# Performance work log

Hardware: AMD Instinct MI355X
Metric: run time of the kernel (lower is better)

## Reference

```python
import jax, jax.numpy as jnp
import numpy as np

N, E = 50000, 800000
IN_DIM, HID, HEADS, EDGE_DIM, OUT_DIM = 329, 64, 4, 2, 1
NEG_SLOPE = 0.2


def setup_inputs() -> dict:
    key = jax.random.key(0)
    ks = jax.random.split(key, 20)
    p = lambda k, shp: (jax.random.normal(k, shp, dtype=jnp.float32) * 0.1)
    inp = {
        'x': jax.random.normal(ks[0], (N, IN_DIM), dtype=jnp.float32),
        'edge_attr': jax.random.normal(ks[1], (E, EDGE_DIM), dtype=jnp.float32),
        'edge_index': jax.random.randint(ks[2], (2, E), 0, N, dtype=jnp.int32),
        # conv1: GATConv(329 -> 64, heads=4, edge_dim=2), concat=True
        'W1': p(ks[3], (IN_DIM, HEADS * HID)),
        'att_src1': p(ks[4], (HEADS, HID)),
        'att_dst1': p(ks[5], (HEADS, HID)),
        'We1': p(ks[6], (EDGE_DIM, HEADS * HID)),
        'att_e1': p(ks[7], (HEADS, HID)),
        'b1': jnp.zeros((HEADS * HID,), jnp.float32),
        # conv2: GATConv(256 -> 64, heads=1, edge_dim=2), concat=True
        'W2': p(ks[8], (HEADS * HID, HID)),
        'att_src2': p(ks[9], (1, HID)),
        'att_dst2': p(ks[10], (1, HID)),
        'We2': p(ks[11], (EDGE_DIM, HID)),
        'att_e2': p(ks[12], (1, HID)),
        'b2': jnp.zeros((HID,), jnp.float32),
        # fc head
        'Wf': p(ks[13], (HID, OUT_DIM)),
        'bf': jnp.zeros((OUT_DIM,), jnp.float32),
    }
    return inp


def gat_conv(x, src, dst, ea, W, att_src, att_dst, We, att_e, bias, heads, out_ch):
    n = x.shape[0]
    h = (x @ W).reshape(n, heads, out_ch)                    # [N,H,C]
    a_src = (h * att_src).sum(-1)                            # [N,H]
    a_dst = (h * att_dst).sum(-1)                            # [N,H]
    e = (ea @ We).reshape(-1, heads, out_ch)                 # [Et,H,C]
    a_e = (e * att_e).sum(-1)                                # [Et,H]
    alpha = a_src[src] + a_dst[dst] + a_e                    # [Et,H]
    alpha = jnp.where(alpha > 0, alpha, NEG_SLOPE * alpha)   # leaky_relu
    amax = jax.ops.segment_max(alpha, dst, num_segments=n)
    ex = jnp.exp(alpha - amax[dst])
    denom = jax.ops.segment_sum(ex, dst, num_segments=n)
    attn = ex / (denom[dst] + 1e-16)                         # [Et,H]
    out = jax.ops.segment_sum(attn[..., None] * h[src], dst, num_segments=n)
    return out.reshape(n, heads * out_ch) + bias


def reference(x, edge_attr, edge_index, W1, att_src1, att_dst1, We1, att_e1, b1,
              W2, att_src2, att_dst2, We2, att_e2, b2, Wf, bf):
    n = x.shape[0]
    # add_self_loops with fill_value='mean' for edge_attr (PyG GATConv default)
    loop = jnp.arange(n, dtype=edge_index.dtype)
    src = jnp.concatenate([edge_index[0], loop])
    dst = jnp.concatenate([edge_index[1], loop])
    mean_ea = jnp.mean(edge_attr, axis=0)
    ea = jnp.concatenate([edge_attr, jnp.broadcast_to(mean_ea, (n, edge_attr.shape[1]))])
    h = gat_conv(x, src, dst, ea, W1, att_src1, att_dst1, We1, att_e1, b1, HEADS, HID)
    h = jax.nn.elu(h)
    h = gat_conv(h, src, dst, ea, W2, att_src2, att_dst2, We2, att_e2, b2, 1, HID)
    out = h @ Wf + bf
    return out.squeeze(-1)
```

## Files before the change

kernel.cpp:

```cpp
#include <hip/hip_runtime.h>
#include <hip/hip_bf16.h>
#include <math.h>


#define DEVFN __device__ __forceinline__

typedef __attribute__((ext_vector_type(8))) short short8;
typedef __attribute__((ext_vector_type(4))) float f32x4;

DEVFN float wave_reduce_sum(float v) {
    for (int off = 32; off; off >>= 1) v += __shfl_xor(v, off);
    return v;
}

DEVFN ushort f2bf_rne(float f) {
    unsigned u = __float_as_uint(f);
    unsigned r = (u + 0x7fff + ((u >> 16) & 1)) >> 16;
    return (ushort)r;
}
DEVFN float bf2f(ushort b) { return __uint_as_float(((unsigned)b) << 16); }

__global__ void k_init(int* __restrict__ deg, float* __restrict__ meanbuf, int N) {
    int i = blockIdx.x * blockDim.x + threadIdx.x;
    if (i < N) deg[i] = 0;
    if (i < 2) meanbuf[i] = 0.f;
}

__global__ void k_count(const int* __restrict__ dstrow, int* __restrict__ deg, int E, int Et) {
    int t = blockIdx.x * blockDim.x + threadIdx.x;
    if (t >= Et) return;
    int d = (t < E) ? dstrow[t] : (t - E);
    atomicAdd(&deg[d], 1);
}

__global__ void k_scan_block(const int* __restrict__ deg, int* __restrict__ rowptr,
                             int* __restrict__ bsums, int N) {
    __shared__ int sd[1024];
    int i = blockIdx.x * 1024 + threadIdx.x;
    sd[threadIdx.x] = (i < N) ? deg[i] : 0;
    __syncthreads();
    for (int off = 1; off < 1024; off <<= 1) {
        int x = (threadIdx.x >= off) ? sd[threadIdx.x - off] : 0;
        __syncthreads();
        sd[threadIdx.x] += x;
        __syncthreads();
    }
    if (i < N) rowptr[i + 1] = sd[threadIdx.x];
    if (threadIdx.x == 1023) bsums[blockIdx.x] = sd[1023];
}

__global__ void k_scan_bsums(const int* __restrict__ bsums, int* __restrict__ boffs, int nb) {
    if (threadIdx.x == 0 && blockIdx.x == 0) {
        int run = 0;
        for (int b = 0; b < nb; b++) { boffs[b] = run; run += bsums[b]; }
    }
}

__global__ void k_scan_finalize(int* __restrict__ rowptr, const int* __restrict__ boffs, int N) {
    int i = blockIdx.x * blockDim.x + threadIdx.x;
    if (i < N) rowptr[i + 1] += boffs[i >> 10];
    if (i == 0) rowptr[0] = 0;
}

__global__ void k_copy_cursor(const int* __restrict__ rowptr, int* __restrict__ cursor, int N) {
    int i = blockIdx.x * blockDim.x + threadIdx.x;
    if (i < N) cursor[i] = rowptr[i];
}

__global__ void k_mean(const float* __restrict__ ea, float* __restrict__ meanbuf, int E) {
    __shared__ float s0s[4], s1s[4];
    float s0 = 0.f, s1 = 0.f;
    for (int i = blockIdx.x * blockDim.x + threadIdx.x; i < E; i += gridDim.x * blockDim.x) {
        float2 v = reinterpret_cast<const float2*>(ea)[i];
        s0 += v.x; s1 += v.y;
    }
    s0 = wave_reduce_sum(s0);
    s1 = wave_reduce_sum(s1);
    int lane = threadIdx.x & 63, w = threadIdx.x >> 6;
    if (lane == 0) { s0s[w] = s0; s1s[w] = s1; }
    __syncthreads();
    if (threadIdx.x == 0) {
        float a = 0.f, b = 0.f;
        for (int i = 0; i < (int)(blockDim.x >> 6); i++) { a += s0s[i]; b += s1s[i]; }
        atomicAdd(&meanbuf[0], a);
        atomicAdd(&meanbuf[1], b);
    }
}

__global__ void k_fill(const int* __restrict__ srcrow, const int* __restrict__ dstrow,
                       int* __restrict__ cursor, int* __restrict__ srcid,
                       float2* __restrict__ ea_csr, const float* __restrict__ ea,
                       const float* __restrict__ meanbuf, float invE, int E, int Et) {
    int t = blockIdx.x * blockDim.x + threadIdx.x;
    if (t >= Et) return;
    int d, s; float2 ev;
    if (t < E) {
        d = dstrow[t]; s = srcrow[t];
        ev = reinterpret_cast<const float2*>(ea)[t];
    } else {
        d = t - E; s = t - E;
        ev = make_float2(meanbuf[0] * invE, meanbuf[1] * invE);
    }
    int pos = atomicAdd(&cursor[d], 1);
    srcid[pos] = s;
    ea_csr[pos] = ev;
}

template <int H>
__global__ void k_collapse(const float* __restrict__ We, const float* __restrict__ att_e,
                           float* __restrict__ M) {
    int t = threadIdx.x;
    int lane = t & 63, w = t >> 6;
    int d = w / H, h = w % H;
    float v = We[(d * H + h) * 64 + lane] * att_e[h * 64 + lane];
    v = wave_reduce_sum(v);
    if (lane == 0) M[d * H + h] = v;
}

__global__ void k_split_wT(const float* __restrict__ W, ushort* __restrict__ hiT,
                           ushort* __restrict__ loT, int K, int Nc, int Kpad) {
    int c = blockIdx.x;
    for (int k = threadIdx.x; k < Kpad; k += blockDim.x) {
        float v = (k < K) ? W[(size_t)k * Nc + c] : 0.f;
        ushort h = f2bf_rne(v);
        ushort l = f2bf_rne(v - bf2f(h));
        hiT[(size_t)c * Kpad + k] = h;
        loT[(size_t)c * Kpad + k] = l;
    }
}

template <int MI, int NI>
__global__ __launch_bounds__(256) void k_gemm_mfma(const float* __restrict__ A,
                                                   const ushort* __restrict__ BhT,
                                                   const ushort* __restrict__ BlT,
                                                   float* __restrict__ C,
                                                   int M, int K, int Kpad, int ldc) {
    constexpr int BM = 32 * MI, BN = 32 * NI;
    constexpr int LDA = 40;
    __shared__ __align__(16) ushort Ah[BM * LDA];
    __shared__ __align__(16) ushort Al[BM * LDA];
    __shared__ __align__(16) ushort Bh[BN * LDA];
    __shared__ __align__(16) ushort Bl[BN * LDA];

    int tid = threadIdx.x, lane = tid & 63, wid = tid >> 6;
    int wr = wid >> 1, wc = wid & 1;
    int bm = blockIdx.x * BM, bn = blockIdx.y * BN;

    f32x4 acc[MI][NI];
#pragma unroll
    for (int mi = 0; mi < MI; ++mi)
#pragma unroll
        for (int ni = 0; ni < NI; ++ni) acc[mi][ni] = (f32x4){0.f, 0.f, 0.f, 0.f};

    int steps = Kpad / 32;
    for (int s = 0; s < steps; ++s) {
        int k0 = s * 32;
        __syncthreads();
#pragma unroll
        for (int j = 0; j < BM / 32; ++j) {
            int slot = tid + 256 * j;
            int row = slot >> 3, ch = slot & 7;
            int gr = bm + row, kb = k0 + ch * 4;
            float v[4];
#pragma unroll
            for (int e = 0; e < 4; ++e) {
                int kk = kb + e;
                v[e] = (gr < M && kk < K) ? A[(size_t)gr * K + kk] : 0.f;
            }
            ushort h[4], l[4];
#pragma unroll
            for (int e = 0; e < 4; ++e) {
                h[e] = f2bf_rne(v[e]);
                l[e] = f2bf_rne(v[e] - bf2f(h[e]));
            }
            *reinterpret_cast<ushort4*>(&Ah[row * LDA + ch * 4]) = make_ushort4(h[0], h[1], h[2], h[3]);
            *reinterpret_cast<ushort4*>(&Al[row * LDA + ch * 4]) = make_ushort4(l[0], l[1], l[2], l[3]);
        }
#pragma unroll
        for (int j = 0; j < BN / 64; ++j) {
            int slot = tid + 256 * j;
            int n = slot >> 2, ch = slot & 3;
            size_t goff = (size_t)(bn + n) * Kpad + k0 + ch * 8;
            *reinterpret_cast<float4*>(&Bh[n * LDA + ch * 8]) =
                *reinterpret_cast<const float4*>(&BhT[goff]);
            *reinterpret_cast<float4*>(&Bl[n * LDA + ch * 8]) =
                *reinterpret_cast<const float4*>(&BlT[goff]);
        }
        __syncthreads();
        int kg = (lane >> 4) * 8;
        int am = wr * (MI * 16) + (lane & 15);
        int bc = wc * (NI * 16) + (lane & 15);
        short8 ah[MI], al[MI], bh[NI], bl[NI];
#pragma unroll
        for (int mi = 0; mi < MI; ++mi) {
            ah[mi] = *reinterpret_cast<const short8*>(&Ah[(am + mi * 16) * LDA + kg]);
            al[mi] = *reinterpret_cast<const short8*>(&Al[(am + mi * 16) * LDA + kg]);
        }
#pragma unroll
        for (int ni = 0; ni < NI; ++ni) {
            bh[ni] = *reinterpret_cast<const short8*>(&Bh[(bc + ni * 16) * LDA + kg]);
            bl[ni] = *reinterpret_cast<const short8*>(&Bl[(bc + ni * 16) * LDA + kg]);
        }
#pragma unroll
        for (int mi = 0; mi < MI; ++mi)
#pragma unroll
            for (int ni = 0; ni < NI; ++ni) {
                acc[mi][ni] = __builtin_amdgcn_mfma_f32_16x16x32_bf16(ah[mi], bh[ni], acc[mi][ni], 0, 0, 0);
                acc[mi][ni] = __builtin_amdgcn_mfma_f32_16x16x32_bf16(ah[mi], bl[ni], acc[mi][ni], 0, 0, 0);
                acc[mi][ni] = __builtin_amdgcn_mfma_f32_16x16x32_bf16(al[mi], bh[ni], acc[mi][ni], 0, 0, 0);
            }
    }
#pragma unroll
    for (int mi = 0; mi < MI; ++mi) {
        int row0 = bm + wr * (MI * 16) + mi * 16 + ((lane >> 4) << 2);
#pragma unroll
        for (int ni = 0; ni < NI; ++ni) {
            int col = bn + wc * (NI * 16) + ni * 16 + (lane & 15);
            f32x4 v = acc[mi][ni];
#pragma unroll
            for (int r = 0; r < 4; ++r)
                if (row0 + r < M) C[(size_t)(row0 + r) * ldc + col] = v[r];
        }
    }
}

template <int H>
__global__ void k_node_attn(const float* __restrict__ h, const float* __restrict__ att_src,
                            const float* __restrict__ att_dst, float* __restrict__ asrc,
                            float* __restrict__ adst, int N) {
    constexpr int HC = H * 64;
    constexpr int NPB = 256 / HC;
    int local = threadIdx.x % HC;
    int n = blockIdx.x * NPB + threadIdx.x / HC;
    if (n >= N) return;
    float v = h[(size_t)n * HC + local];
    float s = v * att_src[local];
    float d = v * att_dst[local];
    for (int off = 32; off; off >>= 1) { s += __shfl_xor(s, off); d += __shfl_xor(d, off); }
    if ((local & 63) == 0) {
        int hh = local >> 6;
        asrc[n * H + hh] = s;
        adst[n * H + hh] = d;
    }
}

template <int H>
__global__ void k_attn(const int* __restrict__ rowptr, const int* __restrict__ srcid,
                       const float2* __restrict__ ea_csr, const float* __restrict__ asrc,
                       const float* __restrict__ adst, const float* __restrict__ M,
                       float* __restrict__ attn, float* __restrict__ dinv, int N) {
    int lane = threadIdx.x & 63;
    int n = blockIdx.x * 4 + (threadIdx.x >> 6);
    if (n >= N) return;
    int start = rowptr[n];
    int items = (rowptr[n + 1] - start) * H;
    int h = lane % H;
    float ad = adst[n * H + h];
    float m0 = M[h], m1 = M[H + h];

    float mx = -1e30f;
    for (int i = lane; i < items; i += 64) {
        int p = start + i / H;
        int s = srcid[p];
        float2 ev = ea_csr[p];
        float al = asrc[s * H + h] + ad + ev.x * m0 + ev.y * m1;
        al = (al > 0.f) ? al : 0.2f * al;
        attn[(size_t)start * H + i] = al;
        mx = fmaxf(mx, al);
    }
    for (int off = H; off < 64; off <<= 1) mx = fmaxf(mx, __shfl_xor(mx, off));

    float ss = 0.f;
    for (int i = lane; i < items; i += 64) {
        float ex = expf(attn[(size_t)start * H + i] - mx);
        attn[(size_t)start * H + i] = ex;
        ss += ex;
    }
    for (int off = H; off < 64; off <<= 1) ss += __shfl_xor(ss, off);
    if (lane < H) dinv[n * H + h] = 1.f / (ss + 1e-16f);
}

template <int H, bool ELU>
__global__ void k_aggregate(const int* __restrict__ rowptr, const int* __restrict__ srcid,
                            const float* __restrict__ attn, const float* __restrict__ dinv,
                            const float4* __restrict__ h4, const float* __restrict__ bias,
                            float4* __restrict__ out4, int N) {
    constexpr int LPN = H * 16;
    constexpr int NPB = 256 / LPN;
    int li = threadIdx.x % LPN;
    int n = blockIdx.x * NPB + threadIdx.x / LPN;
    if (n >= N) return;
    int hh = li >> 4;
    int start = rowptr[n], end = rowptr[n + 1];
    float4 acc = make_float4(0.f, 0.f, 0.f, 0.f);
    int p = start;
    for (; p + 3 < end; p += 4) {
        int s0 = srcid[p], s1 = srcid[p + 1], s2 = srcid[p + 2], s3 = srcid[p + 3];
        float w0 = attn[p * H + hh], w1 = attn[(p + 1) * H + hh];
        float w2 = attn[(p + 2) * H + hh], w3 = attn[(p + 3) * H + hh];
        float4 v0 = h4[(size_t)s0 * LPN + li];
        float4 v1 = h4[(size_t)s1 * LPN + li];
        float4 v2 = h4[(size_t)s2 * LPN + li];
        float4 v3 = h4[(size_t)s3 * LPN + li];
        acc.x += w0 * v0.x + w1 * v1.x + w2 * v2.x + w3 * v3.x;
        acc.y += w0 * v0.y + w1 * v1.y + w2 * v2.y + w3 * v3.y;
        acc.z += w0 * v0.z + w1 * v1.z + w2 * v2.z + w3 * v3.z;
        acc.w += w0 * v0.w + w1 * v1.w + w2 * v2.w + w3 * v3.w;
    }
    for (; p < end; ++p) {
        int s = srcid[p];
        float w = attn[p * H + hh];
        float4 v = h4[(size_t)s * LPN + li];
        acc.x += w * v.x; acc.y += w * v.y; acc.z += w * v.z; acc.w += w * v.w;
    }
    float inv = dinv[n * H + hh];
    float4 b = reinterpret_cast<const float4*>(bias)[li];
    acc.x = acc.x * inv + b.x;
    acc.y = acc.y * inv + b.y;
    acc.z = acc.z * inv + b.z;
    acc.w = acc.w * inv + b.w;
    if (ELU) {
        acc.x = (acc.x > 0.f) ? acc.x : expm1f(acc.x);
        acc.y = (acc.y > 0.f) ? acc.y : expm1f(acc.y);
        acc.z = (acc.z > 0.f) ? acc.z : expm1f(acc.z);
        acc.w = (acc.w > 0.f) ? acc.w : expm1f(acc.w);
    }
    out4[(size_t)n * LPN + li] = acc;
}

__global__ void k_fc(const float* __restrict__ h, const float* __restrict__ Wf,
                     const float* __restrict__ bf, float* __restrict__ out, int N) {
    int lane = threadIdx.x & 63;
    int n = blockIdx.x * 4 + (threadIdx.x >> 6);
    if (n >= N) return;
    float v = h[(size_t)n * 64 + lane] * Wf[lane];
    v = wave_reduce_sum(v);
    if (lane == 0) out[n] = v + bf[0];
}

extern "C" void kernel_launch(void* const* d_in, const int* in_sizes, int n_in,
                              void* d_out, int out_size, void* d_ws, size_t ws_size,
                              hipStream_t stream) {
    const float* x        = (const float*)d_in[0];
    const float* ea       = (const float*)d_in[1];
    const int*   ei       = (const int*)d_in[2];
    const float* W1       = (const float*)d_in[3];
    const float* att_src1 = (const float*)d_in[4];
    const float* att_dst1 = (const float*)d_in[5];
    const float* We1      = (const float*)d_in[6];
    const float* att_e1   = (const float*)d_in[7];
    const float* b1       = (const float*)d_in[8];
    const float* W2       = (const float*)d_in[9];
    const float* att_src2 = (const float*)d_in[10];
    const float* att_dst2 = (const float*)d_in[11];
    const float* We2      = (const float*)d_in[12];
    const float* att_e2   = (const float*)d_in[13];
    const float* b2       = (const float*)d_in[14];
    const float* Wf       = (const float*)d_in[15];
    const float* bf       = (const float*)d_in[16];

    const int IN_DIM = 329;
    const int K1PAD = 352;
    int N  = in_sizes[0] / IN_DIM;
    int E  = in_sizes[1] / 2;
    int Et = E + N;
    const int* srcrow = ei;
    const int* dstrow = ei + E;

    char* p = (char*)d_ws;
    size_t used = 0;
    auto alloc = [&](size_t bytes) -> void* {
        void* r = p;
        size_t pad = (bytes + 255) & ~(size_t)255;
        p += pad; used += pad;
        return r;
    };
    float*  h1     = (float*)alloc((size_t)N * 256 * 4);
    float*  agg1   = (float*)alloc((size_t)N * 256 * 4);
    float*  asrc   = (float*)alloc((size_t)N * 4 * 4);
    float*  adst   = (float*)alloc((size_t)N * 4 * 4);
    float*  dinv   = (float*)alloc((size_t)N * 4 * 4);
    float*  attn   = (float*)alloc((size_t)Et * 4 * 4);
    float2* ea_csr = (float2*)alloc((size_t)Et * 8);
    int*    srcid  = (int*)alloc((size_t)Et * 4);
    ushort* w1hT   = (ushort*)alloc((size_t)256 * K1PAD * 2);
    ushort* w1lT   = (ushort*)alloc((size_t)256 * K1PAD * 2);
    ushort* w2hT   = (ushort*)alloc((size_t)64 * 256 * 2);
    ushort* w2lT   = (ushort*)alloc((size_t)64 * 256 * 2);
    float*  M1     = (float*)alloc(256);
    float*  M2     = (float*)alloc(256);
    float*  meanbuf= (float*)alloc(256);
    int*    rowptr = (int*)alloc((size_t)(N + 1) * 4);
    int*    deg    = (int*)alloc((size_t)N * 4);
    int*    bsums  = (int*)alloc(1024);
    int*    boffs  = (int*)alloc(1024);
    if (used > ws_size) return;

    int gN  = (N + 255) / 256;
    int gEt = (Et + 255) / 256;
    int nb  = (N + 1023) / 1024;
    int gM  = (N + 127) / 128;
    float invE = 1.f / (float)E;

    k_init<<<gN, 256, 0, stream>>>(deg, meanbuf, N);
    k_count<<<gEt, 256, 0, stream>>>(dstrow, deg, E, Et);
    k_scan_block<<<nb, 1024, 0, stream>>>(deg, rowptr, bsums, N);
    k_scan_bsums<<<1, 64, 0, stream>>>(bsums, boffs, nb);
    k_scan_finalize<<<gN, 256, 0, stream>>>(rowptr, boffs, N);
    k_copy_cursor<<<gN, 256, 0, stream>>>(rowptr, deg, N);
    k_mean<<<256, 256, 0, stream>>>(ea, meanbuf, E);
    k_fill<<<gEt, 256, 0, stream>>>(srcrow, dstrow, deg, srcid, ea_csr, ea, meanbuf, invE, E, Et);

    k_collapse<4><<<1, 512, 0, stream>>>(We1, att_e1, M1);
    k_collapse<1><<<1, 128, 0, stream>>>(We2, att_e2, M2);
    k_split_wT<<<256, 384, 0, stream>>>(W1, w1hT, w1lT, IN_DIM, 256, K1PAD);
    k_split_wT<<<64, 256, 0, stream>>>(W2, w2hT, w2lT, 256, 64, 256);

    k_gemm_mfma<4, 4><<<dim3(gM, 2), 256, 0, stream>>>(x, w1hT, w1lT, h1, N, IN_DIM, K1PAD, 256);
    k_node_attn<4><<<N, 256, 0, stream>>>(h1, att_src1, att_dst1, asrc, adst, N);
    k_attn<4><<<(N + 3) / 4, 256, 0, stream>>>(rowptr, srcid, ea_csr, asrc, adst, M1, attn, dinv, N);
    k_aggregate<4, true><<<(N + 3) / 4, 256, 0, stream>>>(rowptr, srcid, attn, dinv,
                                                          (const float4*)h1, b1, (float4*)agg1, N);

    k_gemm_mfma<4, 2><<<dim3(gM, 1), 256, 0, stream>>>(agg1, w2hT, w2lT, h1 , N, 256, 256, 64);
    k_node_attn<1><<<(N + 3) / 4, 256, 0, stream>>>(h1, att_src2, att_dst2, asrc, adst, N);
    k_attn<1><<<(N + 3) / 4, 256, 0, stream>>>(rowptr, srcid, ea_csr, asrc, adst, M2, attn, dinv, N);
    k_aggregate<1, false><<<(N + 15) / 16, 256, 0, stream>>>(rowptr, srcid, attn, dinv,
                                                             (const float4*)h1, b2,
                                                             (float4*)agg1 , N);

    k_fc<<<(N + 3) / 4, 256, 0, stream>>>(agg1, Wf, bf, (float*)d_out, N);
}
```

Baseline: 569.1 us.

## Gather bf16 node features in aggregation and fuse setup kernels

The GEMM epilogue now also writes a bf16 copy of the projected node features. Both aggregation kernels gather that bf16 copy with 16-byte loads of 8 values, which halves the bytes moved by the irregular neighbour gathers. The edge-attribute mean is fused into the degree-count kernel, and the cursor copy is fused into the scan finalize, removing two launches. The trade-off is bf16 rounding error in the aggregated features plus extra epilogue writes and workspace.

```diff
diff --git a/kernel.cpp b/kernel.cpp
--- a/kernel.cpp
+++ b/kernel.cpp
@@ -26,11 +26,30 @@
     if (i < 2) meanbuf[i] = 0.f;
 }
 
-__global__ void k_count(const int* __restrict__ dstrow, int* __restrict__ deg, int E, int Et) {
+__global__ void k_count_mean(const int* __restrict__ dstrow, const float* __restrict__ ea,
+                             int* __restrict__ deg, float* __restrict__ meanbuf, int E, int Et) {
+    __shared__ float s0s[4], s1s[4];
     int t = blockIdx.x * blockDim.x + threadIdx.x;
-    if (t >= Et) return;
-    int d = (t < E) ? dstrow[t] : (t - E);
-    atomicAdd(&deg[d], 1);
+    float s0 = 0.f, s1 = 0.f;
+    if (t < Et) {
+        int d = (t < E) ? dstrow[t] : (t - E);
+        atomicAdd(&deg[d], 1);
+        if (t < E) {
+            float2 v = reinterpret_cast<const float2*>(ea)[t];
+            s0 = v.x; s1 = v.y;
+        }
+    }
+    s0 = wave_reduce_sum(s0);
+    s1 = wave_reduce_sum(s1);
+    int lane = threadIdx.x & 63, w = threadIdx.x >> 6;
+    if (lane == 0) { s0s[w] = s0; s1s[w] = s1; }
+    __syncthreads();
+    if (threadIdx.x == 0) {
+        float a = 0.f, b = 0.f;
+        for (int i = 0; i < (int)(blockDim.x >> 6); i++) { a += s0s[i]; b += s1s[i]; }
+        atomicAdd(&meanbuf[0], a);
+        atomicAdd(&meanbuf[1], b);
+    }
 }
 
 __global__ void k_scan_block(const int* __restrict__ deg, int* __restrict__ rowptr,
@@ -56,35 +75,15 @@
     }
 }
 
-__global__ void k_scan_finalize(int* __restrict__ rowptr, const int* __restrict__ boffs, int N) {
+__global__ void k_scan_finalize(int* __restrict__ rowptr, const int* __restrict__ boffs,
+                                int* __restrict__ cursor, int N) {
     int i = blockIdx.x * blockDim.x + threadIdx.x;
-    if (i < N) rowptr[i + 1] += boffs[i >> 10];
-    if (i == 0) rowptr[0] = 0;
-}
-
-__global__ void k_copy_cursor(const int* __restrict__ rowptr, int* __restrict__ cursor, int N) {
-    int i = blockIdx.x * blockDim.x + threadIdx.x;
-    if (i < N) cursor[i] = rowptr[i];
-}
-
-__global__ void k_mean(const float* __restrict__ ea, float* __restrict__ meanbuf, int E) {
-    __shared__ float s0s[4], s1s[4];
-    float s0 = 0.f, s1 = 0.f;
-    for (int i = blockIdx.x * blockDim.x + threadIdx.x; i < E; i += gridDim.x * blockDim.x) {
-        float2 v = reinterpret_cast<const float2*>(ea)[i];
-        s0 += v.x; s1 += v.y;
-    }
-    s0 = wave_reduce_sum(s0);
-    s1 = wave_reduce_sum(s1);
-    int lane = threadIdx.x & 63, w = threadIdx.x >> 6;
-    if (lane == 0) { s0s[w] = s0; s1s[w] = s1; }
-    __syncthreads();
-    if (threadIdx.x == 0) {
-        float a = 0.f, b = 0.f;
-        for (int i = 0; i < (int)(blockDim.x >> 6); i++) { a += s0s[i]; b += s1s[i]; }
-        atomicAdd(&meanbuf[0], a);
-        atomicAdd(&meanbuf[1], b);
-    }
+    if (i < N) {
+        int val = rowptr[i + 1] + boffs[i >> 10];
+        rowptr[i + 1] = val;
+        if (i + 1 < N) cursor[i + 1] = val;
+    }
+    if (i == 0) { rowptr[0] = 0; cursor[0] = 0; }
 }
 
 __global__ void k_fill(const int* __restrict__ srcrow, const int* __restrict__ dstrow,
@@ -134,6 +133,7 @@
                                                    const ushort* __restrict__ BhT,
                                                    const ushort* __restrict__ BlT,
                                                    float* __restrict__ C,
+                                                   ushort* __restrict__ Cbf,
                                                    int M, int K, int Kpad, int ldc) {
     constexpr int BM = 32 * MI, BN = 32 * NI;
     constexpr int LDA = 40;
@@ -219,7 +219,10 @@
             f32x4 v = acc[mi][ni];
 #pragma unroll
             for (int r = 0; r < 4; ++r)
-                if (row0 + r < M) C[(size_t)(row0 + r) * ldc + col] = v[r];
+                if (row0 + r < M) {
+                    C[(size_t)(row0 + r) * ldc + col] = v[r];
+                    Cbf[(size_t)(row0 + r) * ldc + col] = f2bf_rne(v[r]);
+                }
         }
     }
 }
@@ -281,51 +284,59 @@
 }
 
 template <int H, bool ELU>
-__global__ void k_aggregate(const int* __restrict__ rowptr, const int* __restrict__ srcid,
-                            const float* __restrict__ attn, const float* __restrict__ dinv,
-                            const float4* __restrict__ h4, const float* __restrict__ bias,
-                            float4* __restrict__ out4, int N) {
-    constexpr int LPN = H * 16;
+__global__ void k_aggregate_bf(const int* __restrict__ rowptr, const int* __restrict__ srcid,
+                               const float* __restrict__ attn, const float* __restrict__ dinv,
+                               const ushort* __restrict__ hbf, const float* __restrict__ bias,
+                               float* __restrict__ out, int N) {
+    constexpr int HC = H * 64;
+    constexpr int LPN = HC / 8;
     constexpr int NPB = 256 / LPN;
     int li = threadIdx.x % LPN;
     int n = blockIdx.x * NPB + threadIdx.x / LPN;
     if (n >= N) return;
-    int hh = li >> 4;
+    int hh = li >> 3;
+    const short8* h8 = reinterpret_cast<const short8*>(hbf);
     int start = rowptr[n], end = rowptr[n + 1];
-    float4 acc = make_float4(0.f, 0.f, 0.f, 0.f);
+    float acc[8];
+#pragma unroll
+    for (int j = 0; j < 8; ++j) acc[j] = 0.f;
     int p = start;
     for (; p + 3 < end; p += 4) {
         int s0 = srcid[p], s1 = srcid[p + 1], s2 = srcid[p + 2], s3 = srcid[p + 3];
         float w0 = attn[p * H + hh], w1 = attn[(p + 1) * H + hh];
         float w2 = attn[(p + 2) * H + hh], w3 = attn[(p + 3) * H + hh];
-        float4 v0 = h4[(size_t)s0 * LPN + li];
-        float4 v1 = h4[(size_t)s1 * LPN + li];
-        float4 v2 = h4[(size_t)s2 * LPN + li];
-        float4 v3 = h4[(size_t)s3 * LPN + li];
-        acc.x += w0 * v0.x + w1 * v1.x + w2 * v2.x + w3 * v3.x;
-        acc.y += w0 * v0.y + w1 * v1.y + w2 * v2.y + w3 * v3.y;
-        acc.z += w0 * v0.z + w1 * v1.z + w2 * v2.z + w3 * v3.z;
-        acc.w += w0 * v0.w + w1 * v1.w + w2 * v2.w + w3 * v3.w;
+        short8 v0 = h8[(size_t)s0 * LPN + li];
+        short8 v1 = h8[(size_t)s1 * LPN + li];
+        short8 v2 = h8[(size_t)s2 * LPN + li];
+        short8 v3 = h8[(size_t)s3 * LPN + li];
+#pragma unroll
+        for (int j = 0; j < 8; ++j)
+            acc[j] += w0 * bf2f((ushort)v0[j]) + w1 * bf2f((ushort)v1[j]) +
+                      w2 * bf2f((ushort)v2[j]) + w3 * bf2f((ushort)v3[j]);
     }
     for (; p < end; ++p) {
         int s = srcid[p];
         float w = attn[p * H + hh];
-        float4 v = h4[(size_t)s * LPN + li];
-        acc.x += w * v.x; acc.y += w * v.y; acc.z += w * v.z; acc.w += w * v.w;
+        short8 v = h8[(size_t)s * LPN + li];
+#pragma unroll
+        for (int j = 0; j < 8; ++j) acc[j] += w * bf2f((ushort)v[j]);
     }
     float inv = dinv[n * H + hh];
-    float4 b = reinterpret_cast<const float4*>(bias)[li];
-    acc.x = acc.x * inv + b.x;
-    acc.y = acc.y * inv + b.y;
-    acc.z = acc.z * inv + b.z;
-    acc.w = acc.w * inv + b.w;
-    if (ELU) {
-        acc.x = (acc.x > 0.f) ? acc.x : expm1f(acc.x);
-        acc.y = (acc.y > 0.f) ? acc.y : expm1f(acc.y);
-        acc.z = (acc.z > 0.f) ? acc.z : expm1f(acc.z);
-        acc.w = (acc.w > 0.f) ? acc.w : expm1f(acc.w);
-    }
-    out4[(size_t)n * LPN + li] = acc;
+    const float4* b4 = reinterpret_cast<const float4*>(bias);
+    float4 ba = b4[li * 2], bb = b4[li * 2 + 1];
+    float bv[8] = {ba.x, ba.y, ba.z, ba.w, bb.x, bb.y, bb.z, bb.w};
+    float4 o0, o1;
+    float* ov = &o0.x;
+#pragma unroll
+    for (int j = 0; j < 8; ++j) {
+        float r = acc[j] * inv + bv[j];
+        if (ELU) r = (r > 0.f) ? r : expm1f(r);
+        ((j < 4) ? (&o0.x) : (&o1.x))[j & 3] = r;
+    }
+    (void)ov;
+    float4* out4 = reinterpret_cast<float4*>(out);
+    out4[(size_t)n * (HC / 4) + li * 2]     = o0;
+    out4[(size_t)n * (HC / 4) + li * 2 + 1] = o1;
 }
 
 __global__ void k_fc(const float* __restrict__ h, const float* __restrict__ Wf,
@@ -377,6 +388,8 @@
     };
     float*  h1     = (float*)alloc((size_t)N * 256 * 4);
     float*  agg1   = (float*)alloc((size_t)N * 256 * 4);
+    ushort* h1bf   = (ushort*)alloc((size_t)N * 256 * 2);
+    ushort* h2bf   = (ushort*)alloc((size_t)N * 64 * 2);
     float*  asrc   = (float*)alloc((size_t)N * 4 * 4);
     float*  adst   = (float*)alloc((size_t)N * 4 * 4);
     float*  dinv   = (float*)alloc((size_t)N * 4 * 4);
@@ -403,12 +416,10 @@
     float invE = 1.f / (float)E;
 
     k_init<<<gN, 256, 0, stream>>>(deg, meanbuf, N);
-    k_count<<<gEt, 256, 0, stream>>>(dstrow, deg, E, Et);
+    k_count_mean<<<gEt, 256, 0, stream>>>(dstrow, ea, deg, meanbuf, E, Et);
     k_scan_block<<<nb, 1024, 0, stream>>>(deg, rowptr, bsums, N);
     k_scan_bsums<<<1, 64, 0, stream>>>(bsums, boffs, nb);
-    k_scan_finalize<<<gN, 256, 0, stream>>>(rowptr, boffs, N);
-    k_copy_cursor<<<gN, 256, 0, stream>>>(rowptr, deg, N);
-    k_mean<<<256, 256, 0, stream>>>(ea, meanbuf, E);
+    k_scan_finalize<<<gN, 256, 0, stream>>>(rowptr, boffs, deg , N);
     k_fill<<<gEt, 256, 0, stream>>>(srcrow, dstrow, deg, srcid, ea_csr, ea, meanbuf, invE, E, Et);
 
     k_collapse<4><<<1, 512, 0, stream>>>(We1, att_e1, M1);
@@ -416,18 +427,17 @@
     k_split_wT<<<256, 384, 0, stream>>>(W1, w1hT, w1lT, IN_DIM, 256, K1PAD);
     k_split_wT<<<64, 256, 0, stream>>>(W2, w2hT, w2lT, 256, 64, 256);
 
-    k_gemm_mfma<4, 4><<<dim3(gM, 2), 256, 0, stream>>>(x, w1hT, w1lT, h1, N, IN_DIM, K1PAD, 256);
+    k_gemm_mfma<4, 4><<<dim3(gM, 2), 256, 0, stream>>>(x, w1hT, w1lT, h1, h1bf, N, IN_DIM, K1PAD, 256);
     k_node_attn<4><<<N, 256, 0, stream>>>(h1, att_src1, att_dst1, asrc, adst, N);
     k_attn<4><<<(N + 3) / 4, 256, 0, stream>>>(rowptr, srcid, ea_csr, asrc, adst, M1, attn, dinv, N);
-    k_aggregate<4, true><<<(N + 3) / 4, 256, 0, stream>>>(rowptr, srcid, attn, dinv,
-                                                          (const float4*)h1, b1, (float4*)agg1, N);
-
-    k_gemm_mfma<4, 2><<<dim3(gM, 1), 256, 0, stream>>>(agg1, w2hT, w2lT, h1 , N, 256, 256, 64);
+    k_aggregate_bf<4, true><<<(N + 7) / 8, 256, 0, stream>>>(rowptr, srcid, attn, dinv,
+                                                             h1bf, b1, agg1, N);
+
+    k_gemm_mfma<4, 2><<<dim3(gM, 1), 256, 0, stream>>>(agg1, w2hT, w2lT, h1 , h2bf, N, 256, 256, 64);
     k_node_attn<1><<<(N + 3) / 4, 256, 0, stream>>>(h1, att_src2, att_dst2, asrc, adst, N);
     k_attn<1><<<(N + 3) / 4, 256, 0, stream>>>(rowptr, srcid, ea_csr, asrc, adst, M2, attn, dinv, N);
-    k_aggregate<1, false><<<(N + 15) / 16, 256, 0, stream>>>(rowptr, srcid, attn, dinv,
-                                                             (const float4*)h1, b2,
-                                                             (float4*)agg1 , N);
+    k_aggregate_bf<1, false><<<(N + 31) / 32, 256, 0, stream>>>(rowptr, srcid, attn, dinv,
+                                                                h2bf, b2, agg1 , N);
 
     k_fc<<<(N + 3) / 4, 256, 0, stream>>>(agg1, Wf, bf, (float*)d_out, N);
 }
```

Result: faster. 551.6 us (-3.1%).
